# Optimization experiments

Hardware: AMD Instinct MI355X
Metric: run time of the kernel (lower is better)

## Reference

```python
import jax, jax.numpy as jnp
import numpy as np

B, S, H, D = 2, 2048, 16, 64
HID = H * D
THETA = 10000.0
SCALING_FACTOR = 1
NEG_INF = -1e9


def _rope_cos_sin(position_ids):
    # Llama RoPE: inv_freq over even dims, duplicated halves.
    inv_freq = 1.0 / (THETA ** (jnp.arange(0, D, 2, dtype=jnp.float32) / D))  # [D/2]
    freqs = position_ids.astype(jnp.float32)[..., None] * inv_freq            # [B,S,D/2]
    emb = jnp.concatenate([freqs, freqs], axis=-1)                            # [B,S,D]
    return jnp.cos(emb), jnp.sin(emb)


def _rotate_half(x):
    x1, x2 = jnp.split(x, 2, axis=-1)
    return jnp.concatenate([-x2, x1], axis=-1)


def setup_inputs() -> dict:
    key = jax.random.key(0)
    ks = jax.random.split(key, 6)
    return {
        "hidden_states": jax.random.normal(ks[0], (B, S, HID), dtype=jnp.float32),
        "info_embeddings": jax.random.normal(ks[1], (B, S, HID), dtype=jnp.float32) * 0.1,
        "Wq": jax.random.normal(ks[2], (HID, HID), dtype=jnp.float32) * 0.02,
        "Wk": jax.random.normal(ks[3], (HID, HID), dtype=jnp.float32) * 0.02,
        "Wv": jax.random.normal(ks[4], (HID, HID), dtype=jnp.float32) * 0.02,
        "Wo": jax.random.normal(ks[5], (HID, HID), dtype=jnp.float32) * 0.02,
        "position_ids": jnp.broadcast_to(jnp.arange(S, dtype=jnp.int64), (B, S)),
    }


def reference(hidden_states, info_embeddings, Wq, Wk, Wv, Wo, position_ids):
    b, s, _ = hidden_states.shape
    # projections -> [B,H,S,D]
    q = (hidden_states @ Wq).reshape(b, s, H, D).transpose(0, 2, 1, 3)
    k = (hidden_states @ Wk).reshape(b, s, H, D).transpose(0, 2, 1, 3)
    v = (hidden_states @ Wv).reshape(b, s, H, D).transpose(0, 2, 1, 3)
    # info embedding added to q and k (pre-RoPE)
    info = info_embeddings.reshape(b, s, H, D).transpose(0, 2, 1, 3)
    q = q + info
    k = k + info
    # rotary position embedding
    cos, sin = _rope_cos_sin(position_ids)
    cos = cos[:, None]  # [B,1,S,D]
    sin = sin[:, None]
    q = q * cos + _rotate_half(q) * sin
    k = k * cos + _rotate_half(k) * sin
    # eager attention with custom scaling
    scale = 1.0 / float(np.sqrt(SCALING_FACTOR * D))
    scores = jnp.einsum("bhqd,bhkd->bhqk", q, k) * scale  # [B,H,S,S]
    causal = jnp.tril(jnp.ones((s, s), dtype=bool))
    scores = scores + jnp.where(causal, 0.0, NEG_INF).astype(scores.dtype)
    probs = jax.nn.softmax(scores, axis=-1)  # dropout p=0 (eval)
    attn = jnp.einsum("bhqk,bhkd->bhqd", probs, v)
    attn = attn.transpose(0, 2, 1, 3).reshape(b, s, HID)
    return attn @ Wo
```

## Files before the change

### kernel.cpp

```cpp
#include <hip/hip_runtime.h>
#include <hip/hip_bf16.h>

#define HB 2
#define HS 2048
#define HH 16
#define HD 64
#define HIDN 1024
#define MROWS 4096

typedef __attribute__((ext_vector_type(8))) short s16x8;
typedef __attribute__((ext_vector_type(4))) float f32x4;
typedef unsigned short u16;

__device__ inline u16 f2bf(float f) {
  union { __hip_bfloat16 h; u16 u; } cvt;
  cvt.h = __float2bfloat16(f);
  return cvt.u;
}

__device__ __forceinline__ void gload16(const u16* g, u16* l) {
  __builtin_amdgcn_global_load_lds((const __attribute__((address_space(1))) void*)g,
                                   (__attribute__((address_space(3))) void*)l, 16, 0, 0);
}

__global__ __launch_bounds__(256) void k_cvt(const float* __restrict__ in, u16* __restrict__ out, int n) {
  int i = (blockIdx.x * 256 + threadIdx.x) * 4;
  if (i >= n) return;
  float4 a = *(const float4*)(in + i);
  ushort4 r;
  r.x = f2bf(a.x); r.y = f2bf(a.y); r.z = f2bf(a.z); r.w = f2bf(a.w);
  *(ushort4*)(out + i) = r;
}

__global__ __launch_bounds__(256) void k_transpose(const float* __restrict__ W0, const float* __restrict__ W1,
                                                   const float* __restrict__ W2, const float* __restrict__ W3,
                                                   u16* __restrict__ out) {
  const float* W = (blockIdx.z == 0) ? W0 : (blockIdx.z == 1) ? W1 : (blockIdx.z == 2) ? W2 : W3;
  u16* O = out + (size_t)blockIdx.z * HIDN * HIDN;
  __shared__ float tile[64][65];
  int k0 = blockIdx.y * 64, c0 = blockIdx.x * 64;
  #pragma unroll
  for (int i = 0; i < 16; ++i) {
    int id = threadIdx.x + i * 256;
    int r = id >> 6, c = id & 63;
    tile[r][c] = W[(size_t)(k0 + r) * HIDN + c0 + c];
  }
  __syncthreads();
  #pragma unroll
  for (int i = 0; i < 16; ++i) {
    int id = threadIdx.x + i * 256;
    int r = id >> 6, c = id & 63;
    O[(size_t)(c0 + r) * HIDN + k0 + c] = f2bf(tile[c][r]);
  }
}

#define BM 128
#define BN 128
#define BK 64
#define LDK 72

__global__ __launch_bounds__(256) void k_qkv(const u16* __restrict__ X, const u16* __restrict__ Wt,
                                             const float* __restrict__ info,
                                             u16* __restrict__ Qb, u16* __restrict__ Kb, u16* __restrict__ Vt) {
  __shared__ __align__(16) u16 smem[128 * 136];
  const int z = blockIdx.z;
  const u16* Bt = Wt + (size_t)z * HIDN * HIDN;
  const int tid = threadIdx.x;
  const int lane = tid & 63, wave = tid >> 6;
  const int wr = wave >> 1, wc = wave & 1;
  const int lg = lane >> 4, li = lane & 15;
  const int bm0 = blockIdx.y * BM, bn0 = blockIdx.x * BN;

  const int srow = lane >> 3;
  const int scol = (lane & 7) * 8;

  f32x4 acc[4][4];
  #pragma unroll
  for (int m = 0; m < 4; ++m)
    #pragma unroll
    for (int n = 0; n < 4; ++n) acc[m][n] = (f32x4){0.f, 0.f, 0.f, 0.f};

  for (int k0 = 0; k0 < HIDN; k0 += BK) {
    __syncthreads();
    #pragma unroll
    for (int c = 0; c < 4; ++c) {
      const int ci = wave * 4 + c;
      const int row = ci * 8 + srow;
      gload16(X  + (size_t)(bm0 + row) * HIDN + k0 + scol, &smem[ci * 512]);
      gload16(Bt + (size_t)(bn0 + row) * HIDN + k0 + scol, &smem[8192 + ci * 512]);
    }
    __syncthreads();
    #pragma unroll
    for (int kk = 0; kk < 2; ++kk) {
      s16x8 af[4], bfr[4];
      #pragma unroll
      for (int m = 0; m < 4; ++m) af[m]  = *(const s16x8*)(&smem[(wr * 64 + m * 16 + li) * 64 + kk * 32 + lg * 8]);
      #pragma unroll
      for (int n = 0; n < 4; ++n) bfr[n] = *(const s16x8*)(&smem[8192 + (wc * 64 + n * 16 + li) * 64 + kk * 32 + lg * 8]);
      __builtin_amdgcn_s_setprio(1);
      #pragma unroll
      for (int m = 0; m < 4; ++m)
        #pragma unroll
        for (int n = 0; n < 4; ++n)
          acc[m][n] = __builtin_amdgcn_mfma_f32_16x16x32_bf16(af[m], bfr[n], acc[m][n], 0, 0, 0);
      __builtin_amdgcn_s_setprio(0);
    }
  }

  if (z < 2) {
    u16* dst = (z == 0) ? Qb : Kb;
    #pragma unroll
    for (int m = 0; m < 4; ++m) {
      #pragma unroll
      for (int r = 0; r < 4; ++r) {
        int t = bm0 + wr * 64 + m * 16 + lg * 4 + r;
        int b = t >> 11, s = t & (HS - 1);
        #pragma unroll
        for (int n = 0; n < 2; ++n) {
          int c1 = bn0 + wc * 64 + n * 16 + li;
          float v1 = acc[m][n][r]     + info[(size_t)t * HIDN + c1];
          float v2 = acc[m][n + 2][r] + info[(size_t)t * HIDN + c1 + 32];
          int j = n * 16 + li;
          float invf = exp2f(-0.41524101186092030f * (float)j);
          float ang = (float)s * invf;
          float sn, cs;
          __sincosf(ang, &sn, &cs);
          float o1 = v1 * cs - v2 * sn;
          float o2 = v2 * cs + v1 * sn;
          if (z == 0) { o1 *= 0.18033688011f; o2 *= 0.18033688011f; }
          int h = c1 >> 6, d1 = c1 & 63;
          size_t base = ((size_t)(b * HH + h) * HS + s) * HD;
          dst[base + d1]      = f2bf(o1);
          dst[base + d1 + 32] = f2bf(o2);
        }
      }
    }
  } else {
    __syncthreads();
    #pragma unroll
    for (int m = 0; m < 4; ++m)
      #pragma unroll
      for (int n = 0; n < 4; ++n)
        #pragma unroll
        for (int r = 0; r < 4; ++r) {
          int cl = wc * 64 + n * 16 + li;
          int ml = wr * 64 + m * 16 + lg * 4 + r;
          smem[cl * 136 + ml] = f2bf(acc[m][n][r]);
        }
    __syncthreads();
    const int b = bm0 >> 11, s0 = bm0 & (HS - 1);
    #pragma unroll
    for (int p = 0; p < 8; ++p) {
      int id = tid + p * 256;
      int cl = id >> 4, m8 = (id & 15) * 8;
      int c = bn0 + cl;
      int h = c >> 6, d = c & 63;
      s16x8 v = *(const s16x8*)(&smem[cl * 136 + m8]);
      *(s16x8*)(&Vt[((size_t)(b * HH + h) * HD + d) * HS + s0 + m8]) = v;
    }
  }
}

__global__ __launch_bounds__(256, 3) void k_attn(const u16* __restrict__ Qb, const u16* __restrict__ Kb,
                                                 const u16* __restrict__ Vt, u16* __restrict__ attnOut) {
  __shared__ u16 Ks[2][64 * LDK];
  __shared__ u16 Vs[2][64 * LDK];
  __shared__ u16 Ps[4][16 * LDK];
  const int bidx = blockIdx.x;
  const int bh = bidx & 31;
  const int j  = 31 - (bidx >> 5);
  const int q0 = j * 64;
  const int ntiles = j + 1;

  const u16* Qh = Qb + (size_t)bh * HS * HD;
  const u16* Kh = Kb + (size_t)bh * HS * HD;
  const u16* Vh = Vt + (size_t)bh * HD * HS;
  const int tid = threadIdx.x;
  const int lane = tid & 63, w = tid >> 6;
  const int lg = lane >> 4, li = lane & 15;
  const int b = bh >> 4, h = bh & 15;

  const int row16 = tid >> 3;
  const int col8  = (tid & 7) * 8;

  s16x8 qf[2];
  #pragma unroll
  for (int kk = 0; kk < 2; ++kk)
    qf[kk] = *(const s16x8*)(Qh + (size_t)(q0 + w * 16 + li) * HD + kk * 32 + lg * 8);

  f32x4 o[4];
  #pragma unroll
  for (int n = 0; n < 4; ++n) o[n] = (f32x4){0.f, 0.f, 0.f, 0.f};
  float mrow = -3e38f, lrow = 0.f;

  {
    uint4 ka = *(const uint4*)(Kh + (size_t)row16 * HD + col8);
    uint4 kb = *(const uint4*)(Kh + (size_t)(row16 + 32) * HD + col8);
    uint4 va = *(const uint4*)(Vh + (size_t)row16 * HS + col8);
    uint4 vb = *(const uint4*)(Vh + (size_t)(row16 + 32) * HS + col8);
    *(uint4*)(&Ks[0][row16 * LDK + col8])        = ka;
    *(uint4*)(&Ks[0][(row16 + 32) * LDK + col8]) = kb;
    *(uint4*)(&Vs[0][row16 * LDK + col8])        = va;
    *(uint4*)(&Vs[0][(row16 + 32) * LDK + col8]) = vb;
  }
  __syncthreads();

  for (int t = 0; t < ntiles; ++t) {
    const int cur = t & 1;
    uint4 rKa, rKb, rVa, rVb;
    const bool more = (t + 1 < ntiles);
    if (more) {
      const int kv1 = (t + 1) * 64;
      rKa = *(const uint4*)(Kh + (size_t)(kv1 + row16) * HD + col8);
      rKb = *(const uint4*)(Kh + (size_t)(kv1 + row16 + 32) * HD + col8);
      rVa = *(const uint4*)(Vh + (size_t)row16 * HS + kv1 + col8);
      rVb = *(const uint4*)(Vh + (size_t)(row16 + 32) * HS + kv1 + col8);
    }

    f32x4 sc[4];
    #pragma unroll
    for (int n = 0; n < 4; ++n) sc[n] = (f32x4){0.f, 0.f, 0.f, 0.f};
    __builtin_amdgcn_s_setprio(1);
    #pragma unroll
    for (int kk = 0; kk < 2; ++kk) {
      #pragma unroll
      for (int n = 0; n < 4; ++n) {
        s16x8 kfr = *(const s16x8*)(&Ks[cur][(n * 16 + li) * LDK + kk * 32 + lg * 8]);
        sc[n] = __builtin_amdgcn_mfma_f32_16x16x32_bf16(kfr, qf[kk], sc[n], 0, 0, 0);
      }
    }
    __builtin_amdgcn_s_setprio(0);

    if (t == ntiles - 1) {
      const int qrel = w * 16 + li;
      #pragma unroll
      for (int n = 0; n < 4; ++n)
        #pragma unroll
        for (int r = 0; r < 4; ++r)
          if (n * 16 + lg * 4 + r > qrel) sc[n][r] = -1e9f;
    }

    float pmax = sc[0][0];
    #pragma unroll
    for (int n = 0; n < 4; ++n)
      #pragma unroll
      for (int r = 0; r < 4; ++r) pmax = fmaxf(pmax, sc[n][r]);
    pmax = fmaxf(pmax, __shfl_xor(pmax, 16));
    pmax = fmaxf(pmax, __shfl_xor(pmax, 32));

    if (!__all(pmax - mrow <= 11.5f)) {
      float mnew = fmaxf(mrow, pmax);
      float corr = exp2f(mrow - mnew);
      mrow = mnew;
      lrow *= corr;
      float corrq[4];
      #pragma unroll
      for (int r = 0; r < 4; ++r) corrq[r] = __shfl(corr, lg * 4 + r);
      #pragma unroll
      for (int n = 0; n < 4; ++n)
        #pragma unroll
        for (int r = 0; r < 4; ++r) o[n][r] *= corrq[r];
    }

    float psum = 0.f;
    #pragma unroll
    for (int n = 0; n < 4; ++n) {
      float p0 = exp2f(sc[n][0] - mrow);
      float p1 = exp2f(sc[n][1] - mrow);
      float p2 = exp2f(sc[n][2] - mrow);
      float p3 = exp2f(sc[n][3] - mrow);
      psum += (p0 + p1) + (p2 + p3);
      unsigned a0 = __float_as_uint(p0) + 0x8000u;
      unsigned a1 = __float_as_uint(p1) + 0x8000u;
      unsigned a2 = __float_as_uint(p2) + 0x8000u;
      unsigned a3 = __float_as_uint(p3) + 0x8000u;
      uint2 wv;
      wv.x = __builtin_amdgcn_perm(a1, a0, 0x07060302u);
      wv.y = __builtin_amdgcn_perm(a3, a2, 0x07060302u);
      *(uint2*)(&Ps[w][li * LDK + n * 16 + lg * 4]) = wv;
    }
    psum += __shfl_xor(psum, 16);
    psum += __shfl_xor(psum, 32);
    lrow += psum;

    __builtin_amdgcn_s_setprio(1);
    #pragma unroll
    for (int kk = 0; kk < 2; ++kk) {
      s16x8 pf = *(const s16x8*)(&Ps[w][li * LDK + kk * 32 + lg * 8]);
      #pragma unroll
      for (int n = 0; n < 4; ++n) {
        s16x8 vf = *(const s16x8*)(&Vs[cur][(n * 16 + li) * LDK + kk * 32 + lg * 8]);
        o[n] = __builtin_amdgcn_mfma_f32_16x16x32_bf16(pf, vf, o[n], 0, 0, 0);
      }
    }
    __builtin_amdgcn_s_setprio(0);

    if (more) {
      *(uint4*)(&Ks[cur ^ 1][row16 * LDK + col8])        = rKa;
      *(uint4*)(&Ks[cur ^ 1][(row16 + 32) * LDK + col8]) = rKb;
      *(uint4*)(&Vs[cur ^ 1][row16 * LDK + col8])        = rVa;
      *(uint4*)(&Vs[cur ^ 1][(row16 + 32) * LDK + col8]) = rVb;
      __syncthreads();
    }
  }

  float linv = 1.0f / lrow;
  float linvq[4];
  #pragma unroll
  for (int r = 0; r < 4; ++r) linvq[r] = __shfl(linv, lg * 4 + r);
  #pragma unroll
  for (int n = 0; n < 4; ++n)
    #pragma unroll
    for (int r = 0; r < 4; ++r) {
      int srow = q0 + w * 16 + lg * 4 + r;
      attnOut[(size_t)(b * HS + srow) * HIDN + h * 64 + n * 16 + li] = f2bf(o[n][r] * linvq[r]);
    }
}

__global__ __launch_bounds__(256) void k_out(const u16* __restrict__ A, const u16* __restrict__ Bt,
                                             float* __restrict__ out) {
  __shared__ __align__(16) u16 As[BM * 64];
  __shared__ __align__(16) u16 Bs[BN * 64];
  const int tid = threadIdx.x;
  const int lane = tid & 63, wave = tid >> 6;
  const int wr = wave >> 1, wc = wave & 1;
  const int lg = lane >> 4, li = lane & 15;
  const int bm0 = blockIdx.y * BM, bn0 = blockIdx.x * BN;

  const int srow = lane >> 3;
  const int scol = (lane & 7) * 8;

  f32x4 acc[4][4];
  #pragma unroll
  for (int m = 0; m < 4; ++m)
    #pragma unroll
    for (int n = 0; n < 4; ++n) acc[m][n] = (f32x4){0.f, 0.f, 0.f, 0.f};

  for (int k0 = 0; k0 < HIDN; k0 += BK) {
    __syncthreads();
    #pragma unroll
    for (int c = 0; c < 4; ++c) {
      const int ci = wave * 4 + c;
      const int row = ci * 8 + srow;
      gload16(A  + (size_t)(bm0 + row) * HIDN + k0 + scol, &As[ci * 512]);
      gload16(Bt + (size_t)(bn0 + row) * HIDN + k0 + scol, &Bs[ci * 512]);
    }
    __syncthreads();
    #pragma unroll
    for (int kk = 0; kk < 2; ++kk) {
      s16x8 af[4], bfr[4];
      #pragma unroll
      for (int m = 0; m < 4; ++m) af[m]  = *(const s16x8*)(&As[(wr * 64 + m * 16 + li) * 64 + kk * 32 + lg * 8]);
      #pragma unroll
      for (int n = 0; n < 4; ++n) bfr[n] = *(const s16x8*)(&Bs[(wc * 64 + n * 16 + li) * 64 + kk * 32 + lg * 8]);
      __builtin_amdgcn_s_setprio(1);
      #pragma unroll
      for (int m = 0; m < 4; ++m)
        #pragma unroll
        for (int n = 0; n < 4; ++n)
          acc[m][n] = __builtin_amdgcn_mfma_f32_16x16x32_bf16(af[m], bfr[n], acc[m][n], 0, 0, 0);
      __builtin_amdgcn_s_setprio(0);
    }
  }

  #pragma unroll
  for (int m = 0; m < 4; ++m)
    #pragma unroll
    for (int r = 0; r < 4; ++r) {
      int t = bm0 + wr * 64 + m * 16 + lg * 4 + r;
      #pragma unroll
      for (int n = 0; n < 4; ++n) {
        int c = bn0 + wc * 64 + n * 16 + li;
        out[(size_t)t * HIDN + c] = acc[m][n][r];
      }
    }
}

extern "C" void kernel_launch(void* const* d_in, const int* in_sizes, int n_in,
                              void* d_out, int out_size, void* d_ws, size_t ws_size,
                              hipStream_t stream) {
  const float* hs   = (const float*)d_in[0];
  const float* info = (const float*)d_in[1];
  const float* Wq   = (const float*)d_in[2];
  const float* Wk   = (const float*)d_in[3];
  const float* Wv   = (const float*)d_in[4];
  const float* Wo   = (const float*)d_in[5];
  float* out = (float*)d_out;

  char* ws = (char*)d_ws;
  u16* Xbf  = (u16*)(ws);
  u16* Wt   = (u16*)(ws + ((size_t)8  << 20));
  u16* Qb   = (u16*)(ws + ((size_t)16 << 20));
  u16* Kb   = (u16*)(ws + ((size_t)24 << 20));
  u16* Vt   = (u16*)(ws + ((size_t)32 << 20));
  u16* attn = Xbf;

  k_cvt<<<(MROWS * HIDN / 4 + 255) / 256, 256, 0, stream>>>(hs, Xbf, MROWS * HIDN);
  k_transpose<<<dim3(16, 16, 4), 256, 0, stream>>>(Wq, Wk, Wv, Wo, Wt);
  k_qkv<<<dim3(HIDN / BN, MROWS / BM, 3), 256, 0, stream>>>(Xbf, Wt, info, Qb, Kb, Vt);
  k_attn<<<dim3(1024), 256, 0, stream>>>(Qb, Kb, Vt, attn);
  k_out<<<dim3(HIDN / BN, MROWS / BM), 256, 0, stream>>>(attn, Wt + (size_t)3 * HIDN * HIDN, out);
}
```

Baseline: 125.1 us.

## Single-buffer K/V LDS tiles in attention with register prefetch

Replaces the double-buffered K/V shared-memory tiles with a single buffer. Each iteration stores the prefetched registers, syncs twice, then issues global loads for the next tile, and it drops the occupancy hint of 3 blocks per CU from launch_bounds. This halves K/V LDS use, which could let more blocks fit per CU, at the cost of an extra barrier per tile and less overlap between LDS writes and compute.

```diff
diff --git a/kernel.cpp b/kernel.cpp
--- a/kernel.cpp
+++ b/kernel.cpp
@@ -161,10 +161,10 @@
   }
 }
 
-__global__ __launch_bounds__(256, 3) void k_attn(const u16* __restrict__ Qb, const u16* __restrict__ Kb,
-                                                 const u16* __restrict__ Vt, u16* __restrict__ attnOut) {
-  __shared__ u16 Ks[2][64 * LDK];
-  __shared__ u16 Vs[2][64 * LDK];
+__global__ __launch_bounds__(256) void k_attn(const u16* __restrict__ Qb, const u16* __restrict__ Kb,
+                                              const u16* __restrict__ Vt, u16* __restrict__ attnOut) {
+  __shared__ u16 Ks[64 * LDK];
+  __shared__ u16 Vs[64 * LDK];
   __shared__ u16 Ps[4][16 * LDK];
   const int bidx = blockIdx.x;
   const int bh = bidx & 31;
@@ -193,23 +193,19 @@
   for (int n = 0; n < 4; ++n) o[n] = (f32x4){0.f, 0.f, 0.f, 0.f};
   float mrow = -3e38f, lrow = 0.f;
 
-  {
-    uint4 ka = *(const uint4*)(Kh + (size_t)row16 * HD + col8);
-    uint4 kb = *(const uint4*)(Kh + (size_t)(row16 + 32) * HD + col8);
-    uint4 va = *(const uint4*)(Vh + (size_t)row16 * HS + col8);
-    uint4 vb = *(const uint4*)(Vh + (size_t)(row16 + 32) * HS + col8);
-    *(uint4*)(&Ks[0][row16 * LDK + col8])        = ka;
-    *(uint4*)(&Ks[0][(row16 + 32) * LDK + col8]) = kb;
-    *(uint4*)(&Vs[0][row16 * LDK + col8])        = va;
-    *(uint4*)(&Vs[0][(row16 + 32) * LDK + col8]) = vb;
-  }
-  __syncthreads();
+  uint4 rKa = *(const uint4*)(Kh + (size_t)row16 * HD + col8);
+  uint4 rKb = *(const uint4*)(Kh + (size_t)(row16 + 32) * HD + col8);
+  uint4 rVa = *(const uint4*)(Vh + (size_t)row16 * HS + col8);
+  uint4 rVb = *(const uint4*)(Vh + (size_t)(row16 + 32) * HS + col8);
 
   for (int t = 0; t < ntiles; ++t) {
-    const int cur = t & 1;
-    uint4 rKa, rKb, rVa, rVb;
-    const bool more = (t + 1 < ntiles);
-    if (more) {
+    __syncthreads();
+    *(uint4*)(&Ks[row16 * LDK + col8])        = rKa;
+    *(uint4*)(&Ks[(row16 + 32) * LDK + col8]) = rKb;
+    *(uint4*)(&Vs[row16 * LDK + col8])        = rVa;
+    *(uint4*)(&Vs[(row16 + 32) * LDK + col8]) = rVb;
+    __syncthreads();
+    if (t + 1 < ntiles) {
       const int kv1 = (t + 1) * 64;
       rKa = *(const uint4*)(Kh + (size_t)(kv1 + row16) * HD + col8);
       rKb = *(const uint4*)(Kh + (size_t)(kv1 + row16 + 32) * HD + col8);
@@ -225,7 +221,7 @@
     for (int kk = 0; kk < 2; ++kk) {
       #pragma unroll
       for (int n = 0; n < 4; ++n) {
-        s16x8 kfr = *(const s16x8*)(&Ks[cur][(n * 16 + li) * LDK + kk * 32 + lg * 8]);
+        s16x8 kfr = *(const s16x8*)(&Ks[(n * 16 + li) * LDK + kk * 32 + lg * 8]);
         sc[n] = __builtin_amdgcn_mfma_f32_16x16x32_bf16(kfr, qf[kk], sc[n], 0, 0, 0);
       }
     }
@@ -289,19 +285,11 @@
       s16x8 pf = *(const s16x8*)(&Ps[w][li * LDK + kk * 32 + lg * 8]);
       #pragma unroll
       for (int n = 0; n < 4; ++n) {
-        s16x8 vf = *(const s16x8*)(&Vs[cur][(n * 16 + li) * LDK + kk * 32 + lg * 8]);
+        s16x8 vf = *(const s16x8*)(&Vs[(n * 16 + li) * LDK + kk * 32 + lg * 8]);
         o[n] = __builtin_amdgcn_mfma_f32_16x16x32_bf16(pf, vf, o[n], 0, 0, 0);
       }
     }
     __builtin_amdgcn_s_setprio(0);
-
-    if (more) {
-      *(uint4*)(&Ks[cur ^ 1][row16 * LDK + col8])        = rKa;
-      *(uint4*)(&Ks[cur ^ 1][(row16 + 32) * LDK + col8]) = rKb;
-      *(uint4*)(&Vs[cur ^ 1][row16 * LDK + col8])        = rVa;
-      *(uint4*)(&Vs[cur ^ 1][(row16 + 32) * LDK + col8]) = rVb;
-      __syncthreads();
-    }
   }
 
   float linv = 1.0f / lrow;
```

Result: no change. 125.4 us (+0.3%).
